# Performance work log

Measured on AMD Instinct MI355X. Metric: run time of the kernel, lower is better.

Reference implementation:

```python
import jax, jax.numpy as jnp
import numpy as np

N_HEAD = 32
N_KV = 8
HEAD_DIM = 64  # n_embd // n_head = 2048 // 32
EPS = 1e-6


def bit_linear(x, w):
    """BitNet b1.58 BitLinear (no bias): int8 absmax activation quant (per-token),
    ternary mean-absmax weight quant, straight-through estimator."""
    s = 127.0 / jnp.clip(jnp.max(jnp.abs(x), axis=-1, keepdims=True), 1e-5)
    xq = jnp.clip(jnp.round(x * s), -128.0, 127.0) / s
    xq = x + jax.lax.stop_gradient(xq - x)
    ws = 1.0 / jnp.clip(jnp.mean(jnp.abs(w)), 1e-5)
    wq = jnp.clip(jnp.round(w * ws), -1.0, 1.0) / ws
    wq = w + jax.lax.stop_gradient(wq - w)
    return xq @ wq.T


def sub_ln(x, gamma, beta):
    mean = jnp.mean(x, axis=-1, keepdims=True)
    var = jnp.mean((x - mean) ** 2, axis=-1, keepdims=True)
    return (x - mean) / jnp.sqrt(var + EPS) * gamma + beta


def setup_inputs() -> dict:
    key = jax.random.key(0)
    ks = jax.random.split(key, 8)
    D, KV, F = 2048, 512, 8192
    B, T = 1, 2048
    w_scale = 0.02
    return {
        "x": jax.random.normal(ks[0], (B, T, D), jnp.float32),
        "g1": jnp.ones((D,), jnp.float32),
        "b1": jnp.zeros((D,), jnp.float32),
        "g2": jnp.ones((D,), jnp.float32),
        "b2": jnp.zeros((D,), jnp.float32),
        "wq": jax.random.normal(ks[1], (D, D), jnp.float32) * w_scale,
        "wk": jax.random.normal(ks[2], (KV, D), jnp.float32) * w_scale,
        "wv": jax.random.normal(ks[3], (KV, D), jnp.float32) * w_scale,
        "wo": jax.random.normal(ks[4], (D, D), jnp.float32) * w_scale,
        "w1": jax.random.normal(ks[5], (F, D), jnp.float32) * w_scale,
        "w2": jax.random.normal(ks[6], (D, F), jnp.float32) * w_scale,
    }


def reference(x, g1, b1, g2, b2, wq, wk, wv, wo, w1, w2):
    B, T, D = x.shape
    # --- attention sublayer (pre-norm, residual) ---
    h = sub_ln(x, g1, b1)
    q = bit_linear(h, wq).reshape(B, T, N_HEAD, HEAD_DIM)
    k = bit_linear(h, wk).reshape(B, T, N_KV, HEAD_DIM)
    v = bit_linear(h, wv).reshape(B, T, N_KV, HEAD_DIM)
    rep = N_HEAD // N_KV
    k = jnp.repeat(k, rep, axis=2)  # GQA repeat_interleave
    v = jnp.repeat(v, rep, axis=2)
    attn = jnp.einsum('bqhd,bkhd->bhqk', q, k) * (HEAD_DIM ** -0.5)
    causal = jnp.tril(jnp.ones((T, T), bool))
    attn = jnp.where(causal, attn, -jnp.inf)
    attn = jax.nn.softmax(attn, axis=-1)
    o = jnp.einsum('bhqk,bkhd->bqhd', attn, v).reshape(B, T, D)
    x = x + bit_linear(o, wo)
    # --- FFN sublayer (pre-norm, residual, ReLU^2) ---
    h2 = sub_ln(x, g2, b2)
    f = bit_linear(h2, w1)
    f = jnp.maximum(f, 0.0) ** 2
    return x + bit_linear(f, w2)
```

## Files before the change

### kernel.cpp

```cpp
#include <hip/hip_runtime.h>
#include <hip/hip_bf16.h>
#include <stdint.h>

typedef __bf16 bf16;
typedef signed char i8;
typedef __bf16 v8bf __attribute__((ext_vector_type(8)));
typedef __bf16 v4bf __attribute__((ext_vector_type(4)));
typedef signed char v8i8 __attribute__((ext_vector_type(8)));
typedef int    v4i  __attribute__((ext_vector_type(4)));
typedef float  f32x16 __attribute__((ext_vector_type(16)));

#define MFMA32(a,b,c)   __builtin_amdgcn_mfma_f32_32x32x16_bf16((a),(b),(c),0,0,0)
#define MFMA_I8(a,b,c)  __builtin_amdgcn_mfma_i32_16x16x64_i8((a),(b),(c),0,0,0)

#define INV_D2 (1.0f / 4194304.0f)
#define INV_KV (1.0f / 1048576.0f)
#define INV_F  (1.0f / 16777216.0f)

__device__ __forceinline__ void glds16(const void* g, void* l) {
  __builtin_amdgcn_global_load_lds(
      (const __attribute__((address_space(1))) void*)g,
      (__attribute__((address_space(3))) void*)l, 16, 0, 0);
}

__device__ __forceinline__ float wred_sum(float v) {
#pragma unroll
  for (int o = 32; o; o >>= 1) v += __shfl_xor(v, o);
  return v;
}
__device__ __forceinline__ float wred_max(float v) {
#pragma unroll
  for (int o = 32; o; o >>= 1) v = fmaxf(v, __shfl_xor(v, o));
  return v;
}

__device__ __forceinline__ unsigned int packbf(float a, float b) {
  union { bf16 h[2]; unsigned int u; } x;
  x.h[0] = (bf16)a; x.h[1] = (bf16)b;
  return x.u;
}

__global__ void k_sniff(const unsigned short* __restrict__ x, int* __restrict__ flag) {
  int cnt = 0;
  for (int i = threadIdx.x; i < 2048; i += 64) {
    const unsigned short u = x[i];
    const int e = (u >> 7) & 0xFF;
    if (u == 0 || (e >= 100 && e <= 140)) cnt++;
  }
#pragma unroll
  for (int o = 32; o; o >>= 1) cnt += __shfl_xor(cnt, o);
  if (threadIdx.x == 0) flag[0] = (cnt >= 1844) ? 0 : 1;
}


__global__ void k_zero(float* p, int n) {
  int i = threadIdx.x;
  if (i < n) p[i] = 0.0f;
}

__global__ __launch_bounds__(256) void k_zerof(float4* __restrict__ p) {
  p[(size_t)blockIdx.x * 256 + threadIdx.x] = make_float4(0.f, 0.f, 0.f, 0.f);
}

__global__ __launch_bounds__(256) void k_abssum6(const void* __restrict__ p0, const void* __restrict__ p1,
                                                 const void* __restrict__ p2, const void* __restrict__ p3,
                                                 const void* __restrict__ p4, const void* __restrict__ p5,
                                                 const int* __restrict__ flag, float* __restrict__ out) {
  const int b = blockIdx.x, tid = threadIdx.x;
  const void* w; int seg, base;
  if (b < 64)       { w = p0; seg = 0; base = b; }
  else if (b < 80)  { w = p1; seg = 1; base = b - 64; }
  else if (b < 96)  { w = p2; seg = 2; base = b - 80; }
  else if (b < 160) { w = p3; seg = 3; base = b - 96; }
  else if (b < 416) { w = p4; seg = 4; base = b - 160; }
  else              { w = p5; seg = 5; base = b - 416; }
  const int f32 = flag[0];
  __shared__ float sred[4];
  float s = 0.0f;
  if (f32) {
    const float4* p = (const float4*)w + (size_t)base * 16384;
#pragma unroll 4
    for (int i = 0; i < 64; i++) {
      float4 a = p[i * 256 + tid];
      s += fabsf(a.x) + fabsf(a.y) + fabsf(a.z) + fabsf(a.w);
    }
  } else {
    const v8bf* p = (const v8bf*)w + (size_t)base * 8192;
#pragma unroll 4
    for (int i = 0; i < 32; i++) {
      v8bf v = p[i * 256 + tid];
#pragma unroll
      for (int j = 0; j < 8; j++) s += fabsf((float)v[j]);
    }
  }
  s = wred_sum(s);
  if ((tid & 63) == 0) sred[tid >> 6] = s;
  __syncthreads();
  if (tid == 0) atomicAdd(out + seg, sred[0] + sred[1] + sred[2] + sred[3]);
}

__global__ __launch_bounds__(256) void k_wquant6(const void* __restrict__ p0, const void* __restrict__ p1,
                                                 const void* __restrict__ p2, const void* __restrict__ p3,
                                                 const void* __restrict__ p4, const void* __restrict__ p5,
                                                 i8* __restrict__ d0, i8* __restrict__ d1,
                                                 i8* __restrict__ d2, i8* __restrict__ d3,
                                                 i8* __restrict__ d4, i8* __restrict__ d5,
                                                 const float* __restrict__ wsum,
                                                 const int* __restrict__ flag) {
  const int b = blockIdx.x;
  const void* w; i8* o; int seg, base; float invn;
  if (b < 2048)       { w = p0; o = d0; seg = 0; base = b;         invn = INV_D2; }
  else if (b < 2560)  { w = p1; o = d1; seg = 1; base = b - 2048;  invn = INV_KV; }
  else if (b < 3072)  { w = p2; o = d2; seg = 2; base = b - 2560;  invn = INV_KV; }
  else if (b < 5120)  { w = p3; o = d3; seg = 3; base = b - 3072;  invn = INV_D2; }
  else if (b < 13312) { w = p4; o = d4; seg = 4; base = b - 5120;  invn = INV_F; }
  else                { w = p5; o = d5; seg = 5; base = b - 13312; invn = INV_F; }
  const int gid = base * 256 + threadIdx.x;
  const int i = gid * 8;
  const float ws = 1.0f / fmaxf(wsum[seg] * invn, 1e-5f);
  const int f32 = flag[0];
  float v[8];
  if (f32) {
    float4 a = ((const float4*)w)[gid * 2];
    float4 b4 = ((const float4*)w)[gid * 2 + 1];
    v[0] = a.x; v[1] = a.y; v[2] = a.z; v[3] = a.w;
    v[4] = b4.x; v[5] = b4.y; v[6] = b4.z; v[7] = b4.w;
  } else {
    v8bf t = *(const v8bf*)((const bf16*)w + i);
#pragma unroll
    for (int j = 0; j < 8; j++) v[j] = (float)t[j];
  }
  v8i8 r;
#pragma unroll
  for (int j = 0; j < 8; j++) {
    float t = rintf(v[j] * ws);
    r[j] = (i8)fminf(fmaxf(t, -1.0f), 1.0f);
  }
  *(v8i8*)(o + i) = r;
}

template <bool XINT>
__global__ __launch_bounds__(256) void k_lnq(const void* __restrict__ x, const void* __restrict__ g,
                                             const void* __restrict__ b, i8* __restrict__ q,
                                             float* __restrict__ sc, const int* __restrict__ flag) {
  const int row = blockIdx.x, tid = threadIdx.x;
  const int f32 = flag[0];
  __shared__ float sred[4];
  float v[8];
#pragma unroll
  for (int i = 0; i < 8; i++) {
    const size_t idx = (size_t)row * 2048 + tid + 256 * i;
    if (XINT)      v[i] = ((const float*)x)[idx];
    else if (f32)  v[i] = ((const float*)x)[idx];
    else           v[i] = (float)((const bf16*)x)[idx];
  }
  float s = 0.0f;
#pragma unroll
  for (int i = 0; i < 8; i++) s += v[i];
  s = wred_sum(s);
  if ((tid & 63) == 0) sred[tid >> 6] = s;
  __syncthreads();
  const float mean = (sred[0] + sred[1] + sred[2] + sred[3]) * (1.0f / 2048.0f);
  __syncthreads();
  float vs = 0.0f;
#pragma unroll
  for (int i = 0; i < 8; i++) { float d = v[i] - mean; vs += d * d; }
  vs = wred_sum(vs);
  if ((tid & 63) == 0) sred[tid >> 6] = vs;
  __syncthreads();
  const float rstd = rsqrtf((sred[0] + sred[1] + sred[2] + sred[3]) * (1.0f / 2048.0f) + 1e-6f);
  __syncthreads();
  float hq[8];
  float am = 0.0f;
#pragma unroll
  for (int i = 0; i < 8; i++) {
    const int c = tid + 256 * i;
    const float gv = f32 ? ((const float*)g)[c] : (float)((const bf16*)g)[c];
    const float bv = f32 ? ((const float*)b)[c] : (float)((const bf16*)b)[c];
    hq[i] = (v[i] - mean) * rstd * gv + bv;
    am = fmaxf(am, fabsf(hq[i]));
  }
  am = wred_max(am);
  if ((tid & 63) == 0) sred[tid >> 6] = am;
  __syncthreads();
  am = fmaxf(fmaxf(sred[0], sred[1]), fmaxf(sred[2], sred[3]));
  const float cl = fmaxf(am, 1e-5f);
  const float s127 = 127.0f / cl;
#pragma unroll
  for (int i = 0; i < 8; i++) {
    float r = rintf(hq[i] * s127);
    r = fminf(fmaxf(r, -128.0f), 127.0f);
    q[(size_t)row * 2048 + tid + 256 * i] = (i8)r;
  }
  if (tid == 0) sc[row] = cl * (1.0f / 127.0f);
}

template <int IT>
__global__ __launch_bounds__(256) void k_rowq(const bf16* __restrict__ in, i8* __restrict__ q,
                                              float* __restrict__ sc) {
  const int row = blockIdx.x, tid = threadIdx.x;
  const int C = IT * 256;
  __shared__ float sred[4];
  const bf16* xr = in + (size_t)row * C;
  float v[IT];
  float am = 0.0f;
#pragma unroll
  for (int i = 0; i < IT; i++) {
    v[i] = (float)xr[tid + 256 * i];
    am = fmaxf(am, fabsf(v[i]));
  }
  am = wred_max(am);
  if ((tid & 63) == 0) sred[tid >> 6] = am;
  __syncthreads();
  am = fmaxf(fmaxf(sred[0], sred[1]), fmaxf(sred[2], sred[3]));
  const float cl = fmaxf(am, 1e-5f);
  const float s127 = 127.0f / cl;
#pragma unroll
  for (int i = 0; i < IT; i++) {
    float r = rintf(v[i] * s127);
    r = fminf(fmaxf(r, -128.0f), 127.0f);
    q[(size_t)row * C + tid + 256 * i] = (i8)r;
  }
  if (tid == 0) sc[row] = cl * (1.0f / 127.0f);
}

template <int EPI>
__global__ __launch_bounds__(256) void k_gemm(const i8* __restrict__ A, const i8* __restrict__ B,
                                              const float* __restrict__ sA,
                                              const float* __restrict__ wsum, float winv,
                                              void* __restrict__ out,
                                              int M, int N, int K, int Kc,
                                              const int* __restrict__ flag) {
  __shared__ __align__(16) i8 As[2][128 * 64];
  __shared__ __align__(16) i8 Bs[2][128 * 64];
  const int tid = threadIdx.x;
  const int lane = tid & 63;
  const int ml = lane & 15;
  const int q4 = lane >> 4;
  const int wid = tid >> 6;
  const int wM = wid >> 1;
  const int wN = wid & 1;
  const int m0 = blockIdx.y * 128;
  const int n0 = blockIdx.x * 128;

  const int r0 = tid >> 2;
  const int c0 = (tid & 3) * 16;
  const i8* Ag0 = A + (size_t)(m0 + r0) * K + c0;
  const i8* Ag1 = Ag0 + (size_t)64 * K;
  const i8* Bg0 = B + (size_t)(n0 + r0) * K + c0;
  const i8* Bg1 = Bg0 + (size_t)64 * K;
  const int l0 = wid * 1024;
  const int l1 = 4096 + wid * 1024;

  v4i acc[4][4] = {};

  const int kbeg = blockIdx.z * Kc;
  const int kfin = kbeg + Kc;
  glds16(Ag0 + kbeg, &As[0][l0]);
  glds16(Ag1 + kbeg, &As[0][l1]);
  glds16(Bg0 + kbeg, &Bs[0][l0]);
  glds16(Bg1 + kbeg, &Bs[0][l1]);
  __syncthreads();
  int cb = 0;
  for (int k0 = kbeg; k0 < kfin; k0 += 64) {
    const int kn = k0 + 64;
    if (kn < kfin) {
      glds16(Ag0 + kn, &As[cb ^ 1][l0]);
      glds16(Ag1 + kn, &As[cb ^ 1][l1]);
      glds16(Bg0 + kn, &Bs[cb ^ 1][l0]);
      glds16(Bg1 + kn, &Bs[cb ^ 1][l1]);
    }
    v4i af[4], bfr[4];
#pragma unroll
    for (int i = 0; i < 4; i++) af[i] = *(const v4i*)&As[cb][(wM * 64 + i * 16 + ml) * 64 + q4 * 16];
#pragma unroll
    for (int j = 0; j < 4; j++) bfr[j] = *(const v4i*)&Bs[cb][(wN * 64 + j * 16 + ml) * 64 + q4 * 16];
#pragma unroll
    for (int i = 0; i < 4; i++)
#pragma unroll
      for (int j = 0; j < 4; j++) acc[i][j] = MFMA_I8(af[i], bfr[j], acc[i][j]);
    __syncthreads();
    cb ^= 1;
  }

  if (EPI == 4) {
    int* ob = (int*)out;
#pragma unroll
    for (int i = 0; i < 4; i++)
#pragma unroll
      for (int r = 0; r < 4; r++) {
        const int row = m0 + wM * 64 + i * 16 + q4 * 4 + r;
#pragma unroll
        for (int j = 0; j < 4; j++) {
          const int col = n0 + wN * 64 + j * 16 + ml;
          atomicAdd(ob + (size_t)row * N + col, acc[i][j][r]);
        }
      }
    return;
  }

  const float cw = fmaxf(wsum[0] * winv, 1e-5f);
#pragma unroll
  for (int i = 0; i < 4; i++) {
#pragma unroll
    for (int r = 0; r < 4; r++) {
      const int row = m0 + wM * 64 + i * 16 + q4 * 4 + r;
      const float sa = sA[row] * cw;
#pragma unroll
      for (int j = 0; j < 4; j++) {
        const int col = n0 + wN * 64 + j * 16 + ml;
        const float val = (float)acc[i][j][r] * sa;
        float u = fmaxf(val, 0.0f);
        ((bf16*)out)[(size_t)row * N + col] = (bf16)(u * u);
      }
    }
  }
}

template <int MODE>
__global__ __launch_bounds__(256) void k_epi(const int* __restrict__ acc, int lda, int cofs,
                                             int ncols,
                                             const float* __restrict__ sA,
                                             const float* __restrict__ wsum, float winv,
                                             const void* __restrict__ resid,
                                             void* __restrict__ out,
                                             const int* __restrict__ flag) {
  const int row = blockIdx.x, tid = threadIdx.x;
  const float cw = fmaxf(wsum[0] * winv, 1e-5f);
  const float srow = (MODE == 3) ? cw : sA[row] * cw;
  const int f32 = flag[0];
  for (int c = tid * 4; c < ncols; c += 1024) {
    const v4i a = *(const v4i*)(acc + (size_t)row * lda + cofs + c);
    float s0 = srow, s1 = srow, s2 = srow, s3 = srow;
    if (MODE == 3) {
      float4 sc = *(const float4*)(sA + c);
      s0 *= sc.x; s1 *= sc.y; s2 *= sc.z; s3 *= sc.w;
    }
    const float v0 = (float)a[0] * s0, v1 = (float)a[1] * s1;
    const float v2 = (float)a[2] * s2, v3 = (float)a[3] * s3;
    const size_t o = (size_t)row * ncols + c;
    if (MODE == 0 || MODE == 3) {
      v4bf r;
      r[0] = (bf16)v0; r[1] = (bf16)v1; r[2] = (bf16)v2; r[3] = (bf16)v3;
      *(v4bf*)((bf16*)out + o) = r;
    } else if (MODE == 1) {
      float4 rv;
      if (f32) {
        rv = *(const float4*)((const float*)resid + o);
      } else {
        const v4bf rb = *(const v4bf*)((const bf16*)resid + o);
        rv = make_float4((float)rb[0], (float)rb[1], (float)rb[2], (float)rb[3]);
      }
      *(float4*)((float*)out + o) = make_float4(rv.x + v0, rv.y + v1, rv.z + v2, rv.w + v3);
    } else {
      const float4 rv = *(const float4*)((const float*)resid + o);
      const float o0 = rv.x + v0, o1 = rv.y + v1, o2 = rv.z + v2, o3 = rv.w + v3;
      if (f32) {
        *(float4*)((float*)out + o) = make_float4(o0, o1, o2, o3);
      } else {
        v4bf r;
        r[0] = (bf16)o0; r[1] = (bf16)o1; r[2] = (bf16)o2; r[3] = (bf16)o3;
        *(v4bf*)((bf16*)out + o) = r;
      }
    }
  }
}

__global__ __launch_bounds__(64) void k_attn(const bf16* __restrict__ Q, const bf16* __restrict__ Kb,
                                             const bf16* __restrict__ Vt, bf16* __restrict__ O) {
  const int h = blockIdx.y;
  const int kvh = h >> 2;
  const int t = (blockIdx.x + ((h >> 2) << 3)) & 63;
  const int qw0 = t * 32;
  const int lane = threadIdx.x;
  const int ql = lane & 31;
  const int hi = lane >> 5;

  v8bf qf[4];
  {
    const bf16* qp = Q + (size_t)(qw0 + ql) * 2048 + h * 64 + hi * 8;
#pragma unroll
    for (int c = 0; c < 4; c++) qf[c] = *(const v8bf*)(qp + c * 16);
  }

  float m = -1e30f, l = 0.0f;
  f32x16 acc0 = {}, acc1 = {};

  const bf16* kbase = Kb + kvh * 64 + hi * 8;
  const bf16* vbase = Vt + (size_t)(kvh * 64 + ql) * 2048 + hi * 8;

  for (int kb = 0; kb <= qw0; kb += 32) {
    f32x16 s = {};
    {
      const bf16* kp = kbase + (size_t)(kb + ql) * 512;
#pragma unroll
      for (int c = 0; c < 4; c++) {
        const v8bf kf = *(const v8bf*)(kp + c * 16);
        s = MFMA32(kf, qf[c], s);
      }
    }
    const bool diag = (kb == qw0);
    float p[16];
    float rm = -1e30f;
#pragma unroll
    for (int r = 0; r < 16; r++) {
      float v = s[r] * 0.125f;
      const int koff = (r & 3) + ((r >> 2) << 3) + (hi << 2);
      if (diag && koff > ql) v = -1e30f;
      p[r] = v;
      rm = fmaxf(rm, v);
    }
    rm = fmaxf(rm, __shfl_xor(rm, 32));
    const float mn = fmaxf(m, rm);
    const float alpha = __expf(m - mn);
    m = mn;
    float rs = 0.0f;
#pragma unroll
    for (int r = 0; r < 16; r++) {
      p[r] = __expf(p[r] - mn);
      rs += p[r];
    }
    rs += __shfl_xor(rs, 32);
    l = l * alpha + rs;
#pragma unroll
    for (int r = 0; r < 16; r++) { acc0[r] *= alpha; acc1[r] *= alpha; }

    unsigned int w0 = packbf(p[0], p[1]),   w2 = packbf(p[4], p[5]);
    unsigned int w1 = packbf(p[2], p[3]),   w3 = packbf(p[6], p[7]);
    unsigned int x0 = packbf(p[8], p[9]),   x2 = packbf(p[12], p[13]);
    unsigned int x1 = packbf(p[10], p[11]), x3 = packbf(p[14], p[15]);
    asm("v_permlane32_swap_b32 %0, %1" : "+v"(w0), "+v"(w2));
    asm("v_permlane32_swap_b32 %0, %1" : "+v"(w1), "+v"(w3));
    asm("v_permlane32_swap_b32 %0, %1" : "+v"(x0), "+v"(x2));
    asm("v_permlane32_swap_b32 %0, %1" : "+v"(x1), "+v"(x3));
    union BU { unsigned int u[4]; v8bf v; } B0, B1;
    B0.u[0] = w0; B0.u[1] = w1; B0.u[2] = w2; B0.u[3] = w3;
    B1.u[0] = x0; B1.u[1] = x1; B1.u[2] = x2; B1.u[3] = x3;

    const bf16* vp = vbase + kb;
    const v8bf v00 = *(const v8bf*)(vp);
    const v8bf v01 = *(const v8bf*)(vp + 16);
    const v8bf v10 = *(const v8bf*)(vp + (size_t)32 * 2048);
    const v8bf v11 = *(const v8bf*)(vp + (size_t)32 * 2048 + 16);
    acc0 = MFMA32(v00, B0.v, acc0);
    acc0 = MFMA32(v01, B1.v, acc0);
    acc1 = MFMA32(v10, B0.v, acc1);
    acc1 = MFMA32(v11, B1.v, acc1);
  }

  const float inv = 1.0f / l;
  unsigned int* op = (unsigned int*)(O + (size_t)(qw0 + ql) * 2048 + h * 64);
#pragma unroll
  for (int r = 0; r < 16; r += 2) {
    const int d = (r & 3) + ((r >> 2) << 3) + (hi << 2);
    op[d >> 1] = packbf(acc0[r] * inv, acc0[r + 1] * inv);
    op[(d >> 1) + 16] = packbf(acc1[r] * inv, acc1[r + 1] * inv);
  }
}

extern "C" void kernel_launch(void* const* d_in, const int* in_sizes, int n_in, void* d_out,
                              int out_size, void* d_ws, size_t ws_size, hipStream_t stream) {
  const void* x = d_in[0];
  const void* g1 = d_in[1];
  const void* b1 = d_in[2];
  const void* g2 = d_in[3];
  const void* b2 = d_in[4];
  const void* wq = d_in[5];
  const void* wk = d_in[6];
  const void* wv = d_in[7];
  const void* wo = d_in[8];
  const void* w1 = d_in[9];
  const void* w2 = d_in[10];

  char* ws = (char*)d_ws;
  const size_t MB = 1ull << 20;
  float* wsum = (float*)ws;
  float* s1 = (float*)(ws + 8192);
  float* so = (float*)(ws + 16384);
  float* s2 = (float*)(ws + 24576);
  float* sf = (float*)(ws + 32768);
  int* flag = (int*)(ws + 40960);
  char* big = ws + 65536;

  i8* w1z = (i8*)(big);
  i8* fq  = (i8*)(big);
  i8* w2z = (i8*)(big + 16 * MB);
  i8* wqz = (i8*)(big + 32 * MB);
  i8* wkz = (i8*)(big + 36 * MB);
  i8* wvz = (i8*)(big + 37 * MB);
  i8* woz = (i8*)(big + 38 * MB);
  i8* xq1 = (i8*)(big + 42 * MB);
  i8* oq  = xq1;
  int* accQK = (int*)(big + 46 * MB);
  int* accVt = (int*)(big + 66 * MB);
  bf16* Kbuf = (bf16*)(big + 70 * MB);
  bf16* Vt   = (bf16*)(big + 72 * MB);
  bf16* Qb   = (bf16*)(big + 74 * MB);
  bf16* Ob   = (bf16*)(big + 82 * MB);
  int* accO  = (int*)(big + 46 * MB);
  float* x1  = (float*)(big + 80 * MB);
  i8* xq2 = (i8*)(big + 74 * MB);
  bf16* Fb   = (bf16*)(big + 42 * MB);
  int* accF  = (int*)(big + 42 * MB);

  k_sniff<<<1, 64, 0, stream>>>((const unsigned short*)x, flag);
  k_zero<<<1, 64, 0, stream>>>(wsum, 8);
  k_zerof<<<6144, 256, 0, stream>>>((float4*)accQK);

  k_abssum6<<<672, 256, 0, stream>>>(wq, wk, wv, wo, w1, w2, flag, wsum);
  k_wquant6<<<21504, 256, 0, stream>>>(wq, wk, wv, wo, w1, w2,
                                       wqz, wkz, wvz, woz, w1z, w2z, wsum, flag);

  k_lnq<false><<<2048, 256, 0, stream>>>(x, g1, b1, xq1, s1, flag);
  k_gemm<4><<<dim3(20, 16, 4), 256, 0, stream>>>(xq1, wqz, s1, wsum + 0, INV_D2, accQK,
                                                 2048, 2560, 2048, 512, flag);
  k_gemm<4><<<dim3(16, 4, 4), 256, 0, stream>>>(wvz, xq1, s1, wsum + 2, INV_KV, accVt,
                                                512, 2048, 2048, 512, flag);
  k_epi<0><<<2048, 256, 0, stream>>>(accQK, 2560, 0, 2048, s1, wsum + 0, INV_D2, nullptr, Qb, flag);
  k_epi<0><<<2048, 256, 0, stream>>>(accQK, 2560, 2048, 512, s1, wsum + 1, INV_KV, nullptr, Kbuf, flag);
  k_epi<3><<<512, 256, 0, stream>>>(accVt, 2048, 0, 2048, s1, wsum + 2, INV_KV, nullptr, Vt, flag);
  k_attn<<<dim3(64, 32), 64, 0, stream>>>(Qb, Kbuf, Vt, Ob);
  k_rowq<8><<<2048, 256, 0, stream>>>(Ob, oq, so);
  k_zerof<<<4096, 256, 0, stream>>>((float4*)accO);
  k_gemm<4><<<dim3(16, 16, 4), 256, 0, stream>>>(oq, woz, so, wsum + 3, INV_D2, accO,
                                                 2048, 2048, 2048, 512, flag);
  k_epi<1><<<2048, 256, 0, stream>>>(accO, 2048, 0, 2048, so, wsum + 3, INV_D2, x, x1, flag);

  k_lnq<true><<<2048, 256, 0, stream>>>(x1, g2, b2, xq2, s2, flag);
  k_gemm<2><<<dim3(64, 16, 1), 256, 0, stream>>>(xq2, w1z, s2, wsum + 4, INV_F, Fb,
                                                 2048, 8192, 2048, 2048, flag);
  k_rowq<32><<<2048, 256, 0, stream>>>(Fb, fq, sf);
  k_zerof<<<4096, 256, 0, stream>>>((float4*)accF);
  k_gemm<4><<<dim3(16, 16, 4), 256, 0, stream>>>(fq, w2z, sf, wsum + 5, INV_F, accF,
                                                 2048, 2048, 8192, 2048, flag);
  k_epi<2><<<2048, 256, 0, stream>>>(accF, 2048, 0, 2048, sf, wsum + 5, INV_F, x1, d_out, flag);
}
```

Before: 662.7 us.

## Stage K/V tiles through double-buffered LDS in attention with swizzled blocked layout

The epilogues now write K and V^T into a per-KV-head blocked layout of 32-token tiles with XOR swizzling, and the Q and K epilogues are merged into one kernel. The attention kernel prefetches the next K/V tile into LDS with global_load_lds double buffering, then reads MFMA operands from LDS instead of doing strided global loads. This aims to turn scattered global loads into contiguous asynchronous copies that overlap with compute. It adds LDS use and a vmcnt wait every iteration.

```diff
diff --git a/kernel.cpp b/kernel.cpp
--- a/kernel.cpp
+++ b/kernel.cpp
@@ -327,23 +327,14 @@
                                              const int* __restrict__ flag) {
   const int row = blockIdx.x, tid = threadIdx.x;
   const float cw = fmaxf(wsum[0] * winv, 1e-5f);
-  const float srow = (MODE == 3) ? cw : sA[row] * cw;
+  const float srow = sA[row] * cw;
   const int f32 = flag[0];
   for (int c = tid * 4; c < ncols; c += 1024) {
     const v4i a = *(const v4i*)(acc + (size_t)row * lda + cofs + c);
-    float s0 = srow, s1 = srow, s2 = srow, s3 = srow;
-    if (MODE == 3) {
-      float4 sc = *(const float4*)(sA + c);
-      s0 *= sc.x; s1 *= sc.y; s2 *= sc.z; s3 *= sc.w;
-    }
-    const float v0 = (float)a[0] * s0, v1 = (float)a[1] * s1;
-    const float v2 = (float)a[2] * s2, v3 = (float)a[3] * s3;
+    const float v0 = (float)a[0] * srow, v1 = (float)a[1] * srow;
+    const float v2 = (float)a[2] * srow, v3 = (float)a[3] * srow;
     const size_t o = (size_t)row * ncols + c;
-    if (MODE == 0 || MODE == 3) {
-      v4bf r;
-      r[0] = (bf16)v0; r[1] = (bf16)v1; r[2] = (bf16)v2; r[3] = (bf16)v3;
-      *(v4bf*)((bf16*)out + o) = r;
-    } else if (MODE == 1) {
+    if (MODE == 1) {
       float4 rv;
       if (f32) {
         rv = *(const float4*)((const float*)resid + o);
@@ -366,8 +357,62 @@
   }
 }
 
-__global__ __launch_bounds__(64) void k_attn(const bf16* __restrict__ Q, const bf16* __restrict__ Kb,
-                                             const bf16* __restrict__ Vt, bf16* __restrict__ O) {
+__global__ __launch_bounds__(256) void k_epiQK(const int* __restrict__ acc,
+                                               const float* __restrict__ sA,
+                                               const float* __restrict__ wsum,
+                                               bf16* __restrict__ Qb, bf16* __restrict__ Kh) {
+  const int row = blockIdx.x, tid = threadIdx.x;
+  const float cw0 = fmaxf(wsum[0] * INV_D2, 1e-5f);
+  const float cw1 = fmaxf(wsum[1] * INV_KV, 1e-5f);
+  const float sa = sA[row];
+  bf16* kb_ = Kh + ((size_t)(row >> 5) * 2048) + (row & 31) * 64;
+  const int rx = row & 7;
+  for (int c = tid * 4; c < 2560; c += 1024) {
+    const v4i a = *(const v4i*)(acc + (size_t)row * 2560 + c);
+    if (c < 2048) {
+      v4bf r;
+#pragma unroll
+      for (int j = 0; j < 4; j++) r[j] = (bf16)((float)a[j] * sa * cw0);
+      *(v4bf*)(Qb + (size_t)row * 2048 + c) = r;
+    } else {
+      const int j0 = c - 2048;
+      const int kvh = j0 >> 6, d = j0 & 63;
+      v4bf r;
+#pragma unroll
+      for (int j = 0; j < 4; j++) r[j] = (bf16)((float)a[j] * sa * cw1);
+      const int elem = ((((d >> 3) ^ rx) << 3) + (d & 7));
+      *(v4bf*)(kb_ + (size_t)kvh * 131072 + elem) = r;
+    }
+  }
+}
+
+__global__ __launch_bounds__(256) void k_epiVt(const int* __restrict__ acc,
+                                               const float* __restrict__ sT,
+                                               const float* __restrict__ wsum,
+                                               bf16* __restrict__ Vtb) {
+  const int vr = blockIdx.x, tid = threadIdx.x;
+  const int kvh = vr >> 6, dd = vr & 63;
+  const float cw = fmaxf(wsum[2] * INV_KV, 1e-5f);
+  const int sw = (dd >> 1) & 3;
+  bf16* vb = Vtb + (size_t)kvh * 131072 + dd * 32;
+  for (int c = tid * 4; c < 2048; c += 1024) {
+    const v4i a = *(const v4i*)(acc + (size_t)vr * 2048 + c);
+    const float4 sc = *(const float4*)(sT + c);
+    v4bf r;
+    r[0] = (bf16)((float)a[0] * sc.x * cw);
+    r[1] = (bf16)((float)a[1] * sc.y * cw);
+    r[2] = (bf16)((float)a[2] * sc.z * cw);
+    r[3] = (bf16)((float)a[3] * sc.w * cw);
+    const int tq = c & 31;
+    const int elem = (c >> 5) * 2048 + ((((tq >> 3) ^ sw) << 3) + (tq & 7));
+    *(v4bf*)(vb + elem) = r;
+  }
+}
+
+__global__ __launch_bounds__(64) void k_attn(const bf16* __restrict__ Q, const bf16* __restrict__ Kh,
+                                             const bf16* __restrict__ Vtb, bf16* __restrict__ O) {
+  __shared__ __align__(16) bf16 Kl[2][2048];
+  __shared__ __align__(16) bf16 Vl[2][2048];
   const int h = blockIdx.y;
   const int kvh = h >> 2;
   const int t = (blockIdx.x + ((h >> 2) << 3)) & 63;
@@ -386,16 +431,33 @@
   float m = -1e30f, l = 0.0f;
   f32x16 acc0 = {}, acc1 = {};
 
-  const bf16* kbase = Kb + kvh * 64 + hi * 8;
-  const bf16* vbase = Vt + (size_t)(kvh * 64 + ql) * 2048 + hi * 8;
+  const bf16* khead = Kh + (size_t)kvh * 131072 + lane * 8;
+  const bf16* vhead = Vtb + (size_t)kvh * 131072 + lane * 8;
+
+#pragma unroll
+  for (int cc = 0; cc < 4; cc++) {
+    glds16(khead + cc * 512, &Kl[0][cc * 512]);
+    glds16(vhead + cc * 512, &Vl[0][cc * 512]);
+  }
+  asm volatile("s_waitcnt vmcnt(0)" ::: "memory");
+  int cb = 0;
 
   for (int kb = 0; kb <= qw0; kb += 32) {
+    if (kb + 32 <= qw0) {
+      const int tb = ((kb + 32) >> 5) * 2048;
+#pragma unroll
+      for (int cc = 0; cc < 4; cc++) {
+        glds16(khead + tb + cc * 512, &Kl[cb ^ 1][cc * 512]);
+        glds16(vhead + tb + cc * 512, &Vl[cb ^ 1][cc * 512]);
+      }
+    }
     f32x16 s = {};
     {
-      const bf16* kp = kbase + (size_t)(kb + ql) * 512;
+      const char* kl = (const char*)&Kl[cb][0] + ql * 128;
 #pragma unroll
       for (int c = 0; c < 4; c++) {
-        const v8bf kf = *(const v8bf*)(kp + c * 16);
+        const int sl = ((2 * c + hi) ^ (ql & 7)) << 4;
+        const v8bf kf = *(const v8bf*)(kl + sl);
         s = MFMA32(kf, qf[c], s);
       }
     }
@@ -437,15 +499,22 @@
     B0.u[0] = w0; B0.u[1] = w1; B0.u[2] = w2; B0.u[3] = w3;
     B1.u[0] = x0; B1.u[1] = x1; B1.u[2] = x2; B1.u[3] = x3;
 
-    const bf16* vp = vbase + kb;
-    const v8bf v00 = *(const v8bf*)(vp);
-    const v8bf v01 = *(const v8bf*)(vp + 16);
-    const v8bf v10 = *(const v8bf*)(vp + (size_t)32 * 2048);
-    const v8bf v11 = *(const v8bf*)(vp + (size_t)32 * 2048 + 16);
-    acc0 = MFMA32(v00, B0.v, acc0);
-    acc0 = MFMA32(v01, B1.v, acc0);
-    acc1 = MFMA32(v10, B0.v, acc1);
-    acc1 = MFMA32(v11, B1.v, acc1);
+    {
+      const char* vl = (const char*)&Vl[cb][0] + ql * 64;
+      const int sx = (ql >> 1) & 3;
+      const int sl0 = ((0 + hi) ^ sx) << 4;
+      const int sl1 = ((2 + hi) ^ sx) << 4;
+      const v8bf v00 = *(const v8bf*)(vl + sl0);
+      const v8bf v01 = *(const v8bf*)(vl + sl1);
+      const v8bf v10 = *(const v8bf*)(vl + 2048 + sl0);
+      const v8bf v11 = *(const v8bf*)(vl + 2048 + sl1);
+      acc0 = MFMA32(v00, B0.v, acc0);
+      acc0 = MFMA32(v01, B1.v, acc0);
+      acc1 = MFMA32(v10, B0.v, acc1);
+      acc1 = MFMA32(v11, B1.v, acc1);
+    }
+    asm volatile("s_waitcnt vmcnt(0)" ::: "memory");
+    cb ^= 1;
   }
 
   const float inv = 1.0f / l;
@@ -493,8 +562,8 @@
   i8* oq  = xq1;
   int* accQK = (int*)(big + 46 * MB);
   int* accVt = (int*)(big + 66 * MB);
-  bf16* Kbuf = (bf16*)(big + 70 * MB);
-  bf16* Vt   = (bf16*)(big + 72 * MB);
+  bf16* Kh   = (bf16*)(big + 70 * MB);
+  bf16* Vtb  = (bf16*)(big + 72 * MB);
   bf16* Qb   = (bf16*)(big + 74 * MB);
   bf16* Ob   = (bf16*)(big + 82 * MB);
   int* accO  = (int*)(big + 46 * MB);
@@ -516,10 +585,9 @@
                                                  2048, 2560, 2048, 512, flag);
   k_gemm<4><<<dim3(16, 4, 4), 256, 0, stream>>>(wvz, xq1, s1, wsum + 2, INV_KV, accVt,
                                                 512, 2048, 2048, 512, flag);
-  k_epi<0><<<2048, 256, 0, stream>>>(accQK, 2560, 0, 2048, s1, wsum + 0, INV_D2, nullptr, Qb, flag);
-  k_epi<0><<<2048, 256, 0, stream>>>(accQK, 2560, 2048, 512, s1, wsum + 1, INV_KV, nullptr, Kbuf, flag);
-  k_epi<3><<<512, 256, 0, stream>>>(accVt, 2048, 0, 2048, s1, wsum + 2, INV_KV, nullptr, Vt, flag);
-  k_attn<<<dim3(64, 32), 64, 0, stream>>>(Qb, Kbuf, Vt, Ob);
+  k_epiQK<<<2048, 256, 0, stream>>>(accQK, s1, wsum, Qb, Kh);
+  k_epiVt<<<512, 256, 0, stream>>>(accVt, s1, wsum, Vtb);
+  k_attn<<<dim3(64, 32), 64, 0, stream>>>(Qb, Kh, Vtb, Ob);
   k_rowq<8><<<2048, 256, 0, stream>>>(Ob, oq, so);
   k_zerof<<<4096, 256, 0, stream>>>((float4*)accO);
   k_gemm<4><<<dim3(16, 16, 4), 256, 0, stream>>>(oq, woz, so, wsum + 3, INV_D2, accO,
```

New measurement: 657.1 us. About the same (-0.8%).
